# Kernel optimization log

Measured on AMD Instinct MI355X. Metric: run time of the kernel, lower is better.

The kernel has to match this reference:

```python
import jax, jax.numpy as jnp
import numpy as np

B, S, D, H, R, N, KR = 2, 2048, 1024, 16, 256, 8, 128
DH = D // H
EPS = 1e-5


def setup_inputs() -> dict:
    key = jax.random.key(0)
    ks = jax.random.split(key, 20)
    sm = lambda k, n: jax.nn.softmax(jax.random.normal(k, (B, S, n), jnp.float32), axis=-1)
    return {
        "x": jax.random.normal(ks[0], (B, S, D), jnp.float32),
        "fqk_w_Q": sm(ks[1], N),
        "fqk_w_K": sm(ks[2], N),
        "fv_w": sm(ks[3], N),
        "rqk_w_Q": sm(ks[4], N),
        "rqk_w_K": sm(ks[5], N),
        "rv_w": sm(ks[6], N),
        "feature_know_w": sm(ks[7], N),
        "restore_know_w": sm(ks[8], N),
        "f_qk": jax.random.normal(ks[9], (N, D, R), jnp.float32) * 0.02,
        "f_v": jax.random.normal(ks[10], (N, D, R), jnp.float32) * 0.02,
        "r_qk": jax.random.normal(ks[11], (N, R, D), jnp.float32) * 0.02,
        "r_v": jax.random.normal(ks[12], (N, R, D), jnp.float32) * 0.02,
        "f_know": jax.random.normal(ks[13], (N, D, KR), jnp.float32) * 0.02,
        "r_know": jax.random.normal(ks[14], (N, KR, D), jnp.float32) * 0.02,
        "W_O": jax.random.normal(ks[15], (D, D), jnp.float32) * 0.02,
        "ln1_g": jnp.ones((D,), jnp.float32),
        "ln1_b": jnp.zeros((D,), jnp.float32),
        "ln2_g": jnp.ones((D,), jnp.float32),
        "ln2_b": jnp.zeros((D,), jnp.float32),
    }


def _layernorm(x, g, b):
    m = jnp.mean(x, axis=-1, keepdims=True)
    v = jnp.mean(jnp.square(x - m), axis=-1, keepdims=True)
    return (x - m) * jax.lax.rsqrt(v + EPS) * g + b


def _feature(x, neurons, w):
    # fused form of einsum('bsd,ndr->bsnr') + einsum('bsnr,bsn->bsr')
    return jnp.einsum('bsd,bsn,ndr->bsr', x, w, neurons)


def _restore(h, neurons, w):
    # fused form of einsum('bsr,nrd->bsnd') + einsum('bsnd,bsn->bsd')
    return jnp.einsum('bsr,bsn,nrd->bsd', h, w, neurons)


def _causal_sdpa(q, k, v):
    # q,k,v: [B,H,S,DH]
    scores = jnp.einsum('bhqd,bhkd->bhqk', q, k) / jnp.sqrt(jnp.float32(DH))
    mask = jnp.tril(jnp.ones((S, S), bool))
    scores = jnp.where(mask, scores, jnp.finfo(scores.dtype).min)
    p = jax.nn.softmax(scores, axis=-1)
    return jnp.einsum('bhqk,bhkd->bhqd', p, v)


def _block(x, fqk_w_Q, fqk_w_K, fv_w, rqk_w_Q, rqk_w_K, rv_w,
           feature_know_w, restore_know_w, f_qk, f_v, r_qk, r_v,
           f_know, r_know, W_O, ln1_g, ln1_b, ln2_g, ln2_b):
    nx = _layernorm(x, ln1_g, ln1_b)
    h_q = _feature(nx, f_qk, fqk_w_Q)
    h_k = _feature(nx, f_qk, fqk_w_K)
    h_v = _feature(nx, f_v, fv_w)
    Q = _restore(h_q, r_qk, rqk_w_Q)
    K = _restore(h_k, r_qk, rqk_w_K)
    V = _restore(h_v, r_v, rv_w)
    to_heads = lambda t: t.reshape(B, S, H, DH).transpose(0, 2, 1, 3)
    attn = _causal_sdpa(to_heads(Q), to_heads(K), to_heads(V))
    attn = attn.transpose(0, 2, 1, 3).reshape(B, S, D)
    attn_out = attn @ W_O.T  # nn.Linear(d_model,d_model,bias=False)
    x = x + attn_out
    nx2 = _layernorm(x, ln2_g, ln2_b)
    h = _feature(nx2, f_know, feature_know_w)
    know_out = _restore(h, r_know, restore_know_w)
    return x + know_out


def reference(x, fqk_w_Q, fqk_w_K, fv_w, rqk_w_Q, rqk_w_K, rv_w,
              feature_know_w, restore_know_w, f_qk, f_v, r_qk, r_v,
              f_know, r_know, W_O, ln1_g, ln1_b, ln2_g, ln2_b):
    return _block(x, fqk_w_Q, fqk_w_K, fv_w, rqk_w_Q, rqk_w_K, rv_w,
                  feature_know_w, restore_know_w, f_qk, f_v, r_qk, r_v,
                  f_know, r_know, W_O, ln1_g, ln1_b, ln2_g, ln2_b)
```

## Files before the change

### kernel.cpp

```cpp
#include <hip/hip_runtime.h>
#include <hip/hip_bf16.h>


typedef __bf16 bf16_t;
typedef __bf16 bf16x4 __attribute__((ext_vector_type(4)));
typedef __bf16 bf16x8 __attribute__((ext_vector_type(8)));
typedef float f32x4 __attribute__((ext_vector_type(4)));

#define B_DIM 2
#define S_LEN 2048
#define D_DIM 1024
#define H_NUM 16
#define DH 64
#define N_NEU 8
#define R_DIM 256
#define KR_DIM 128
#define ROWS (B_DIM * S_LEN)

static __device__ __forceinline__ void gl_lds16(const void* g, void* l)
{
    __builtin_amdgcn_global_load_lds(
        (__attribute__((address_space(1))) void*)(g),
        (__attribute__((address_space(3))) void*)(l), 16, 0, 0);
}

__global__ __launch_bounds__(256)
void tcast_kernel(const float* __restrict__ in, bf16_t* __restrict__ out, int I, int J)
{
    __shared__ float t[32][33];
    const int bJ = blockIdx.x * 32, bI = blockIdx.y * 32;
    const size_t boff = (size_t)blockIdx.z * I * J;
    const int tx = threadIdx.x, ty = threadIdx.y;
#pragma unroll
    for (int i = 0; i < 4; i++)
        t[ty * 4 + i][tx] = in[boff + (size_t)(bI + ty * 4 + i) * J + bJ + tx];
    __syncthreads();
#pragma unroll
    for (int i = 0; i < 4; i++)
        out[boff + (size_t)(bJ + ty * 4 + i) * I + bI + tx] = (bf16_t)t[tx][ty * 4 + i];
}

__global__ __launch_bounds__(256)
void tbf_kernel(const bf16_t* __restrict__ in, bf16_t* __restrict__ out, int I, int J)
{
    __shared__ bf16_t t[32][33];
    const int bJ = blockIdx.x * 32, bI = blockIdx.y * 32;
    const size_t boff = (size_t)blockIdx.z * I * J;
    const int tx = threadIdx.x, ty = threadIdx.y;
#pragma unroll
    for (int i = 0; i < 4; i++)
        t[ty * 4 + i][tx] = in[boff + (size_t)(bI + ty * 4 + i) * J + bJ + tx];
    __syncthreads();
#pragma unroll
    for (int i = 0; i < 4; i++)
        out[boff + (size_t)(bJ + ty * 4 + i) * I + bI + tx] = t[tx][ty * 4 + i];
}

__global__ __launch_bounds__(256)
void cast_kernel(const float* __restrict__ in, bf16_t* __restrict__ out, int n4)
{
    int i = blockIdx.x * 256 + threadIdx.x;
    if (i < n4) {
        float4 v = ((const float4*)in)[i];
        bf16_t* op = out + (size_t)i * 4;
        op[0] = (bf16_t)v.x; op[1] = (bf16_t)v.y; op[2] = (bf16_t)v.z; op[3] = (bf16_t)v.w;
    }
}

__global__ __launch_bounds__(256)
void ln_kernel(const float* __restrict__ x, const float* __restrict__ g,
               const float* __restrict__ beta, bf16_t* __restrict__ out)
{
    __shared__ float red[4];
    const int row = blockIdx.x;
    const int tid = threadIdx.x;
    float4 v = *(const float4*)&x[(size_t)row * D_DIM + tid * 4];

    float s = v.x + v.y + v.z + v.w;
#pragma unroll
    for (int o = 32; o; o >>= 1) s += __shfl_down(s, o);
    if ((tid & 63) == 0) red[tid >> 6] = s;
    __syncthreads();
    float mean = (red[0] + red[1] + red[2] + red[3]) * (1.f / D_DIM);
    __syncthreads();

    float dx = v.x - mean, dy = v.y - mean, dz = v.z - mean, dw = v.w - mean;
    float q = dx * dx + dy * dy + dz * dz + dw * dw;
#pragma unroll
    for (int o = 32; o; o >>= 1) q += __shfl_down(q, o);
    if ((tid & 63) == 0) red[tid >> 6] = q;
    __syncthreads();
    float var = (red[0] + red[1] + red[2] + red[3]) * (1.f / D_DIM);
    float rstd = rsqrtf(var + 1e-5f);

    float4 gv = *(const float4*)&g[tid * 4];
    float4 bv = *(const float4*)&beta[tid * 4];
    bf16_t* op = out + (size_t)row * D_DIM + tid * 4;
    op[0] = (bf16_t)(dx * rstd * gv.x + bv.x);
    op[1] = (bf16_t)(dy * rstd * gv.y + bv.y);
    op[2] = (bf16_t)(dz * rstd * gv.z + bv.z);
    op[3] = (bf16_t)(dw * rstd * gv.w + bv.w);
}

__global__ __launch_bounds__(256)
void ln2x_kernel(const float* __restrict__ x, const bf16_t* __restrict__ P0,
                 const bf16_t* __restrict__ P1, const float* __restrict__ g,
                 const float* __restrict__ beta, float* __restrict__ outf,
                 bf16_t* __restrict__ outn)
{
    __shared__ float red[4];
    const int row = blockIdx.x;
    const int tid = threadIdx.x;
    const size_t base = (size_t)row * D_DIM + tid * 4;
    float4 v  = *(const float4*)&x[base];
    bf16x4 p0 = *(const bf16x4*)&P0[base];
    bf16x4 p1 = *(const bf16x4*)&P1[base];
    v.x += (float)p0[0] + (float)p1[0];
    v.y += (float)p0[1] + (float)p1[1];
    v.z += (float)p0[2] + (float)p1[2];
    v.w += (float)p0[3] + (float)p1[3];
    *(float4*)&outf[base] = v;

    float s = v.x + v.y + v.z + v.w;
#pragma unroll
    for (int o = 32; o; o >>= 1) s += __shfl_down(s, o);
    if ((tid & 63) == 0) red[tid >> 6] = s;
    __syncthreads();
    float mean = (red[0] + red[1] + red[2] + red[3]) * (1.f / D_DIM);
    __syncthreads();

    float dx = v.x - mean, dy = v.y - mean, dz = v.z - mean, dw = v.w - mean;
    float q = dx * dx + dy * dy + dz * dz + dw * dw;
#pragma unroll
    for (int o = 32; o; o >>= 1) q += __shfl_down(q, o);
    if ((tid & 63) == 0) red[tid >> 6] = q;
    __syncthreads();
    float var = (red[0] + red[1] + red[2] + red[3]) * (1.f / D_DIM);
    float rstd = rsqrtf(var + 1e-5f);

    float4 gv = *(const float4*)&g[tid * 4];
    float4 bv = *(const float4*)&beta[tid * 4];
    bf16_t* op = outn + base;
    op[0] = (bf16_t)(dx * rstd * gv.x + bv.x);
    op[1] = (bf16_t)(dy * rstd * gv.y + bv.y);
    op[2] = (bf16_t)(dz * rstd * gv.z + bv.z);
    op[3] = (bf16_t)(dw * rstd * gv.w + bv.w);
}

__global__ __launch_bounds__(256)
void wsf_kernel(const bf16_t* __restrict__ y,
                const float* __restrict__ wfQ, const float* __restrict__ wrQ,
                const float* __restrict__ wfK, const float* __restrict__ wrK,
                const float* __restrict__ wfV, const float* __restrict__ wrV,
                bf16_t* __restrict__ sq, bf16_t* __restrict__ sk, bf16_t* __restrict__ sv)
{
    const int r = threadIdx.x;
    const int row = blockIdx.x;
    const bf16_t* yrow = y + (size_t)row * 4096;
    const float* fQ = wfQ + row * N_NEU;
    const float* fK = wfK + row * N_NEU;
    const float* fV = wfV + row * N_NEU;
    float aQ = 0.f, aK = 0.f, aV = 0.f;
#pragma unroll
    for (int n = 0; n < N_NEU; n++) {
        float yq = (float)yrow[n * R_DIM + r];
        float yv = (float)yrow[2048 + n * R_DIM + r];
        aQ += fQ[n] * yq;
        aK += fK[n] * yq;
        aV += fV[n] * yv;
    }
    const float* rQ = wrQ + row * N_NEU;
    const float* rK = wrK + row * N_NEU;
    const float* rV = wrV + row * N_NEU;
    const size_t rb = (size_t)row * 2048;
#pragma unroll
    for (int n = 0; n < N_NEU; n++) {
        sq[rb + n * R_DIM + r] = (bf16_t)(rQ[n] * aQ);
        sk[rb + n * R_DIM + r] = (bf16_t)(rK[n] * aK);
        sv[rb + n * R_DIM + r] = (bf16_t)(rV[n] * aV);
    }
}

__global__ __launch_bounds__(256)
void ws2_kernel(const bf16_t* __restrict__ P0, const bf16_t* __restrict__ P1,
                const float* __restrict__ wf, const float* __restrict__ wr,
                bf16_t* __restrict__ sout)
{
    const int lr = threadIdx.x >> 7;
    const int r  = threadIdx.x & 127;
    const int row = blockIdx.x * 2 + lr;
    const size_t rb = (size_t)row * (N_NEU * KR_DIM);
    const float* wfp = wf + row * N_NEU;
    const float* wrp = wr + row * N_NEU;
    float acc = 0.f;
#pragma unroll
    for (int n = 0; n < N_NEU; n++) {
        size_t i = rb + n * KR_DIM + r;
        acc += wfp[n] * ((float)P0[i] + (float)P1[i]);
    }
    bf16_t* srow = sout + rb;
#pragma unroll
    for (int n = 0; n < N_NEU; n++) srow[n * KR_DIM + r] = (bf16_t)(wrp[n] * acc);
}

template<int EPI>
__global__ __launch_bounds__(512, 2)
void gemm256_kernel(const bf16_t* __restrict__ A, const bf16_t* __restrict__ Bt,
                    const bf16_t* __restrict__ Bt2, int splitMy,
                    void* Cout, int M, int N, int K)
{
    __shared__ bf16_t As[3][256][32];
    __shared__ bf16_t Bs[3][128][32];
    const int tid = threadIdx.x;
    const int l = tid & 63, w = tid >> 6;
    const int wr = w >> 1, wc = w & 1;

    const int nbxy = gridDim.x * gridDim.y;
    int bid = blockIdx.y * gridDim.x + blockIdx.x;
    if ((nbxy & 7) == 0) bid = (bid & 7) * (nbxy >> 3) + (bid >> 3);
    const int bx = bid % gridDim.x, by = bid / gridDim.x;

    const int m0 = by * 256, n0 = bx * 128;
    const bf16_t* Bsel = (by < splitMy) ? Bt : Bt2;

    int kbeg = 0, kend = K;
    if constexpr (EPI == 2) { const int half = K >> 1; kbeg = blockIdx.z * half; kend = kbeg + half; }

    const int strow  = w * 16 + (l >> 2);
    const int scelem = ((((l & 3) * 16) ^ ((strow & 6) << 3)) >> 1);
    const bf16_t* Ag0 = A    + (size_t)(m0 + strow) * K + scelem;
    const bf16_t* Ag1 = A    + (size_t)(m0 + strow + 128) * K + scelem;
    const bf16_t* Bg0 = Bsel + (size_t)(n0 + strow) * K + scelem;

    auto stage = [&](int buf, int k0) {
        char* dA = (char*)&As[buf][0][0] + w * 1024;
        char* dB = (char*)&Bs[buf][0][0] + w * 1024;
        gl_lds16(Ag0 + k0, dA);
        gl_lds16(Ag1 + k0, dA + 8192);
        gl_lds16(Bg0 + k0, dB);
    };

    f32x4 acc[4][4];
    const f32x4 zero = {0.f, 0.f, 0.f, 0.f};
#pragma unroll
    for (int i = 0; i < 4; i++)
#pragma unroll
        for (int j = 0; j < 4; j++) acc[i][j] = zero;

    const int fr  = l & 15;
    const int fkb = (l >> 4) * 16;

    stage(0, kbeg);
    stage(1, kbeg + 32);

    const int nK = (kend - kbeg) >> 5;
    for (int it = 0; it < nK; ++it) {
        if (it + 1 < nK) {
            asm volatile("s_waitcnt vmcnt(3)" ::: "memory");
        } else {
            asm volatile("s_waitcnt vmcnt(0)" ::: "memory");
        }
        __builtin_amdgcn_s_barrier();
        __builtin_amdgcn_sched_barrier(0);

        const int cur = it % 3;
        const char* Ab = (const char*)&As[cur][0][0];
        const char* Bb = (const char*)&Bs[cur][0][0];
        bf16x8 af[4], bv[4];
#pragma unroll
        for (int i = 0; i < 4; i++) {
            const int rowA = wr * 64 + i * 16 + fr;
            af[i] = *(const bf16x8*)(Ab + rowA * 64 + (fkb ^ ((rowA & 6) << 3)));
        }
#pragma unroll
        for (int i = 0; i < 4; i++) {
            const int rowB = wc * 64 + i * 16 + fr;
            bv[i] = *(const bf16x8*)(Bb + rowB * 64 + (fkb ^ ((rowB & 6) << 3)));
        }

        if (it + 2 < nK) stage((it + 2) % 3, kbeg + (it + 2) * 32);

        __builtin_amdgcn_s_setprio(1);
#pragma unroll
        for (int mi = 0; mi < 4; mi++)
#pragma unroll
            for (int ni = 0; ni < 4; ni++)
                acc[mi][ni] = __builtin_amdgcn_mfma_f32_16x16x32_bf16(af[mi], bv[ni], acc[mi][ni], 0, 0, 0);
        __builtin_amdgcn_s_setprio(0);
    }

    const int orow = (l >> 4) * 4;
    const int ocol = l & 15;
#pragma unroll
    for (int mi = 0; mi < 4; mi++)
#pragma unroll
        for (int ni = 0; ni < 4; ni++)
#pragma unroll
            for (int j = 0; j < 4; j++) {
                int row = m0 + wr * 64 + mi * 16 + orow + j;
                int col = n0 + wc * 64 + ni * 16 + ocol;
                size_t idx = (size_t)row * N + col;
                if constexpr (EPI == 0) {
                    ((bf16_t*)Cout)[idx] = (bf16_t)acc[mi][ni][j];
                } else {
                    ((bf16_t*)Cout)[(size_t)blockIdx.z * M * N + idx] = (bf16_t)acc[mi][ni][j];
                }
            }
}

template<int EPI>
__global__ __launch_bounds__(256)
void gemm_kernel(const bf16_t* __restrict__ A, const bf16_t* __restrict__ Bt,
                 const bf16_t* __restrict__ Bt2, int splitMy,
                 void* Cout, const float* resid, int M, int N, int K)
{
    __shared__ bf16_t As[3][128][32];
    __shared__ bf16_t Bs[3][128][32];
    const int tid = threadIdx.x;
    const int l = tid & 63, w = tid >> 6;
    const int wr = w >> 1, wc = w & 1;

    const int nbxy = gridDim.x * gridDim.y;
    int bid = blockIdx.y * gridDim.x + blockIdx.x;
    if ((nbxy & 7) == 0) bid = (bid & 7) * (nbxy >> 3) + (bid >> 3);
    const int bx = bid % gridDim.x, by = bid / gridDim.x;

    const int m0 = by * 128, n0 = bx * 128;
    const bf16_t* Bsel = (by < splitMy) ? Bt : Bt2;

    const int kbeg = 0, kend = K;

    const int srow = l >> 2;
    const int scolswz = (((l & 3) * 16) ^ ((srow & 6) << 3)) >> 1;
    const bf16_t* Ag0 = A    + (size_t)(m0 + w * 32 + srow) * K + scolswz;
    const bf16_t* Ag1 = Ag0 + (size_t)16 * K;
    const bf16_t* Bg0 = Bsel + (size_t)(n0 + w * 32 + srow) * K + scolswz;
    const bf16_t* Bg1 = Bg0 + (size_t)16 * K;

    auto stage = [&](int buf, int k0) {
        char* Asb = (char*)&As[buf][0][0] + w * 2048;
        char* Bsb = (char*)&Bs[buf][0][0] + w * 2048;
        gl_lds16(Ag0 + k0, Asb);
        gl_lds16(Ag1 + k0, Asb + 1024);
        gl_lds16(Bg0 + k0, Bsb);
        gl_lds16(Bg1 + k0, Bsb + 1024);
    };

    f32x4 acc[4][4];
    const f32x4 zero = {0.f, 0.f, 0.f, 0.f};
#pragma unroll
    for (int i = 0; i < 4; i++)
#pragma unroll
        for (int j = 0; j < 4; j++) acc[i][j] = zero;

    const int fr = l & 15;
    const int fkb = (l >> 4) * 16;

    stage(0, kbeg);
    stage(1, kbeg + 32);

    const int nK = (kend - kbeg) >> 5;
    for (int it = 0; it < nK; ++it) {
        if (it + 1 < nK) {
            asm volatile("s_waitcnt vmcnt(4)" ::: "memory");
        } else {
            asm volatile("s_waitcnt vmcnt(0)" ::: "memory");
        }
        __builtin_amdgcn_s_barrier();
        __builtin_amdgcn_sched_barrier(0);

        const int cur = it % 3;
        const char* Ab = (const char*)&As[cur][0][0];
        const char* Bb = (const char*)&Bs[cur][0][0];
        bf16x8 af[4], bv[4];
#pragma unroll
        for (int i = 0; i < 4; i++) {
            const int rowA = wr * 64 + i * 16 + fr;
            af[i] = *(const bf16x8*)(Ab + rowA * 64 + (fkb ^ ((rowA & 6) << 3)));
        }
#pragma unroll
        for (int i = 0; i < 4; i++) {
            const int rowB = wc * 64 + i * 16 + fr;
            bv[i] = *(const bf16x8*)(Bb + rowB * 64 + (fkb ^ ((rowB & 6) << 3)));
        }

        if (it + 2 < nK) stage((it + 2) % 3, kbeg + (it + 2) * 32);

        __builtin_amdgcn_s_setprio(1);
#pragma unroll
        for (int mi = 0; mi < 4; mi++)
#pragma unroll
            for (int ni = 0; ni < 4; ni++)
                acc[mi][ni] = __builtin_amdgcn_mfma_f32_16x16x32_bf16(af[mi], bv[ni], acc[mi][ni], 0, 0, 0);
        __builtin_amdgcn_s_setprio(0);
    }

    const int orow = (l >> 4) * 4;
    const int ocol = l & 15;
#pragma unroll
    for (int mi = 0; mi < 4; mi++)
#pragma unroll
        for (int ni = 0; ni < 4; ni++)
#pragma unroll
            for (int j = 0; j < 4; j++) {
                int row = m0 + wr * 64 + mi * 16 + orow + j;
                int col = n0 + wc * 64 + ni * 16 + ocol;
                size_t idx = (size_t)row * N + col;
                if constexpr (EPI == 0) {
                    ((bf16_t*)Cout)[idx] = (bf16_t)acc[mi][ni][j];
                } else {
                    ((float*)Cout)[idx] = acc[mi][ni][j] + resid[idx];
                }
            }
}

__global__ __launch_bounds__(256, 4)
void fa_kernel(const bf16_t* __restrict__ Q, const bf16_t* __restrict__ K,
               const bf16_t* __restrict__ Vt, bf16_t* __restrict__ O)
{
    __shared__ bf16_t Ks[2][64][64];
    __shared__ bf16_t Vs[2][64][64];
    __shared__ bf16_t Ps[4][16][64];

    const int tid = threadIdx.x;
    const int l = tid & 63, w = tid >> 6;

    const int bid  = blockIdx.x;
    const int xcd  = bid & 7;
    const int slot = bid >> 3;
    const int head = slot & 3;
    const int j5   = slot >> 2;
    const int t5   = j5 & 7, u5 = j5 >> 3;
    const int qb   = 8 * u5 + ((u5 & 1) ? (7 - t5) : t5);
    const int bh   = xcd * 4 + head;
    const int b = bh >> 4, h = bh & 15;
    const int q0 = qb * 64;
    const int nt = qb + 1;

    const bf16_t* Qp = Q + (size_t)b * S_LEN * D_DIM + h * DH;
    const bf16_t* Kp = K + (size_t)b * S_LEN * D_DIM + h * DH;
    const bf16_t* Vp = Vt + (size_t)b * D_DIM * S_LEN + (size_t)h * DH * S_LEN;

    const int fr = l & 15, fg = l >> 4, fk = fg * 8;
    const int srow = tid >> 2;
    const int scel = (tid & 3) * 16;
    const int swz  = (srow & 7) << 4;
    const bf16_t* Kst = Kp + (size_t)srow * D_DIM + scel;
    const bf16_t* Vst = Vp + (size_t)srow * S_LEN + scel;

    bf16x8 ones8;
#pragma unroll
    for (int i = 0; i < 8; i++) ones8[i] = (bf16_t)1.f;

    const f32x4 zero = {0.f, 0.f, 0.f, 0.f};
    const float C_LOG2 = 0.125f * 1.44269504f;

    bf16x8 qf[2];
#pragma unroll
    for (int ks = 0; ks < 2; ks++)
        qf[ks] = *(const bf16x8*)(Qp + (size_t)(q0 + w * 16 + fr) * D_DIM + ks * 32 + fk);

    f32x4 o[4];
    f32x4 la = zero;
    float m_r[4];
#pragma unroll
    for (int j = 0; j < 4; j++) { o[j] = zero; m_r[j] = -1e30f; }

    uint4 ka = *(const uint4*)(Kst);
    uint4 kb = *(const uint4*)(Kst + 8);
    uint4 va = *(const uint4*)(Vst);
    uint4 vb = *(const uint4*)(Vst + 8);
    {
        char* kd = (char*)&Ks[0][srow][0];
        char* vd = (char*)&Vs[0][srow][0];
        *(uint4*)(kd + ((scel * 2)      ^ swz)) = ka;
        *(uint4*)(kd + ((scel * 2 + 16) ^ swz)) = kb;
        *(uint4*)(vd + ((scel * 2)      ^ swz)) = va;
        *(uint4*)(vd + ((scel * 2 + 16) ^ swz)) = vb;
    }
    if (nt > 1) {
        ka = *(const uint4*)(Kst + (size_t)64 * D_DIM);
        kb = *(const uint4*)(Kst + (size_t)64 * D_DIM + 8);
        va = *(const uint4*)(Vst + 64);
        vb = *(const uint4*)(Vst + 64 + 8);
    }
    __syncthreads();

    for (int t = 0; t < nt; t++) {
        const int cur = t & 1;

        if (t + 1 < nt) {
            char* kd = (char*)&Ks[cur ^ 1][srow][0];
            char* vd = (char*)&Vs[cur ^ 1][srow][0];
            *(uint4*)(kd + ((scel * 2)      ^ swz)) = ka;
            *(uint4*)(kd + ((scel * 2 + 16) ^ swz)) = kb;
            *(uint4*)(vd + ((scel * 2)      ^ swz)) = va;
            *(uint4*)(vd + ((scel * 2 + 16) ^ swz)) = vb;
        }
        if (t + 2 < nt) {
            const size_t kn = (size_t)(t + 2) * 64;
            ka = *(const uint4*)(Kst + kn * D_DIM);
            kb = *(const uint4*)(Kst + kn * D_DIM + 8);
            va = *(const uint4*)(Vst + kn);
            vb = *(const uint4*)(Vst + kn + 8);
        }

        const int k0 = t * 64;
        f32x4 sc[4];
#pragma unroll
        for (int ni = 0; ni < 4; ni++) sc[ni] = zero;
        __builtin_amdgcn_s_setprio(1);
#pragma unroll
        for (int ks = 0; ks < 2; ks++) {
#pragma unroll
            for (int ni = 0; ni < 4; ni++) {
                const int row = ni * 16 + fr;
                bf16x8 kf = *(const bf16x8*)((const char*)&Ks[cur][row][0]
                              + ((ks * 64 + fg * 16) ^ ((fr & 7) << 4)));
                sc[ni] = __builtin_amdgcn_mfma_f32_16x16x32_bf16(qf[ks], kf, sc[ni], 0, 0, 0);
            }
        }
        __builtin_amdgcn_s_setprio(0);

        float p[4][4];
        if (t == qb) {
#pragma unroll
            for (int ni = 0; ni < 4; ni++) {
                const int key = k0 + ni * 16 + fr;
#pragma unroll
                for (int j = 0; j < 4; j++) {
                    const int qg = q0 + w * 16 + fg * 4 + j;
                    p[ni][j] = (key <= qg) ? sc[ni][j] * C_LOG2 : -1e30f;
                }
            }
        } else {
#pragma unroll
            for (int ni = 0; ni < 4; ni++)
#pragma unroll
                for (int j = 0; j < 4; j++)
                    p[ni][j] = sc[ni][j] * C_LOG2;
        }

#pragma unroll
        for (int j = 0; j < 4; j++) {
            float rmax = fmaxf(fmaxf(p[0][j], p[1][j]), fmaxf(p[2][j], p[3][j]));
#pragma unroll
            for (int d = 1; d < 16; d <<= 1) rmax = fmaxf(rmax, __shfl_xor(rmax, d));
            if (rmax > m_r[j] + 8.f) {
                float scale = exp2f(m_r[j] - rmax);
                la[j] *= scale;
#pragma unroll
                for (int nc = 0; nc < 4; nc++) o[nc][j] *= scale;
                m_r[j] = rmax;
            }
#pragma unroll
            for (int ni = 0; ni < 4; ni++)
                p[ni][j] = exp2f(p[ni][j] - m_r[j]);
        }

#pragma unroll
        for (int ni = 0; ni < 4; ni++)
#pragma unroll
            for (int j = 0; j < 4; j++) {
                const int qrow = fg * 4 + j;
                char* pd = (char*)&Ps[w][qrow][0];
                *(bf16_t*)(pd + (((ni * 16 + fr) * 2) ^ ((qrow & 7) << 4))) = (bf16_t)p[ni][j];
            }

        __builtin_amdgcn_s_setprio(1);
#pragma unroll
        for (int ks = 0; ks < 2; ks++) {
            bf16x8 pa = *(const bf16x8*)((const char*)&Ps[w][fr][0]
                          + ((ks * 64 + fg * 16) ^ ((fr & 7) << 4)));
            la = __builtin_amdgcn_mfma_f32_16x16x32_bf16(pa, ones8, la, 0, 0, 0);
#pragma unroll
            for (int nc = 0; nc < 4; nc++) {
                const int row = nc * 16 + fr;
                bf16x8 vf = *(const bf16x8*)((const char*)&Vs[cur][row][0]
                              + ((ks * 64 + fg * 16) ^ ((fr & 7) << 4)));
                o[nc] = __builtin_amdgcn_mfma_f32_16x16x32_bf16(pa, vf, o[nc], 0, 0, 0);
            }
        }
        __builtin_amdgcn_s_setprio(0);

        __syncthreads();
    }

#pragma unroll
    for (int j = 0; j < 4; j++) {
        const float inv = 1.f / la[j];
        const int q = q0 + w * 16 + fg * 4 + j;
        bf16_t* op = O + (size_t)(b * S_LEN + q) * D_DIM + h * DH;
#pragma unroll
        for (int nc = 0; nc < 4; nc++)
            op[nc * 16 + fr] = (bf16_t)(o[nc][j] * inv);
    }
}

extern "C" void kernel_launch(void* const* d_in, const int* in_sizes, int n_in,
                              void* d_out, int out_size, void* d_ws, size_t ws_size,
                              hipStream_t stream)
{
    const float* x      = (const float*)d_in[0];
    const float* fqk_wQ = (const float*)d_in[1];
    const float* fqk_wK = (const float*)d_in[2];
    const float* fv_w   = (const float*)d_in[3];
    const float* rqk_wQ = (const float*)d_in[4];
    const float* rqk_wK = (const float*)d_in[5];
    const float* rv_w   = (const float*)d_in[6];
    const float* fkn_w  = (const float*)d_in[7];
    const float* rkn_w  = (const float*)d_in[8];
    const float* f_qk   = (const float*)d_in[9];
    const float* f_v    = (const float*)d_in[10];
    const float* r_qk   = (const float*)d_in[11];
    const float* r_v    = (const float*)d_in[12];
    const float* f_know = (const float*)d_in[13];
    const float* r_know = (const float*)d_in[14];
    const float* W_O    = (const float*)d_in[15];
    const float* ln1g   = (const float*)d_in[16];
    const float* ln1b   = (const float*)d_in[17];
    const float* ln2g   = (const float*)d_in[18];
    const float* ln2b   = (const float*)d_in[19];
    float* out_f = (float*)d_out;
    (void)ws_size; (void)in_sizes; (void)n_in; (void)out_size;

    char* ws = (char*)d_ws;
    const size_t MB = 1024 * 1024;
    bf16_t* rqkT   = (bf16_t*)(ws + 0 * MB);
    bf16_t* rvT    = (bf16_t*)(ws + 4 * MB);
    bf16_t* rknT   = (bf16_t*)(ws + 8 * MB);
    bf16_t* woB    = (bf16_t*)(ws + 10 * MB);
    bf16_t* fknT   = (bf16_t*)(ws + 12 * MB);
    bf16_t* buf_nx = (bf16_t*)(ws + 14 * MB);
    bf16_t* buf_y  = (bf16_t*)(ws + 22 * MB);
    char*   buf_s  = ws + 54 * MB;
    bf16_t* fqkT   = (bf16_t*)(buf_s);
    bf16_t* fvT    = (bf16_t*)(buf_s + 4 * MB);
    bf16_t* s_q    = (bf16_t*)(buf_s);
    bf16_t* s_k    = (bf16_t*)(buf_s) + (size_t)4096 * 2048;
    bf16_t* s_v    = (bf16_t*)(buf_s) + (size_t)8192 * 2048;
    bf16_t* attn   = (bf16_t*)(buf_s);
    bf16_t* P0     = (bf16_t*)(buf_s + 16 * MB);
    bf16_t* P0k    = (bf16_t*)(buf_s);
    bf16_t* sk2    = (bf16_t*)(buf_s + 32 * MB);
    bf16_t* Qb     = buf_y;
    bf16_t* Kb     = buf_y + (size_t)4096 * 1024;
    bf16_t* Vb     = buf_y + (size_t)8192 * 1024;
    bf16_t* Vt     = buf_nx;

    const dim3 blk256(256), blk512(512), blkT(32, 8);

    tcast_kernel<<<dim3(R_DIM / 32, D_DIM / 32, N_NEU), blkT, 0, stream>>>(f_qk, fqkT, D_DIM, R_DIM);
    tcast_kernel<<<dim3(R_DIM / 32, D_DIM / 32, N_NEU), blkT, 0, stream>>>(f_v, fvT, D_DIM, R_DIM);
    tcast_kernel<<<dim3(KR_DIM / 32, D_DIM / 32, N_NEU), blkT, 0, stream>>>(f_know, fknT, D_DIM, KR_DIM);
    tcast_kernel<<<dim3(D_DIM / 32, 2048 / 32, 1), blkT, 0, stream>>>(r_qk, rqkT, 2048, D_DIM);
    tcast_kernel<<<dim3(D_DIM / 32, 2048 / 32, 1), blkT, 0, stream>>>(r_v, rvT, 2048, D_DIM);
    tcast_kernel<<<dim3(D_DIM / 32, 1024 / 32, 1), blkT, 0, stream>>>(r_know, rknT, 1024, D_DIM);
    cast_kernel<<<dim3(1024 * 1024 / 4 / 256), blk256, 0, stream>>>(W_O, woB, 1024 * 1024 / 4);

    ln_kernel<<<dim3(ROWS), blk256, 0, stream>>>(x, ln1g, ln1b, buf_nx);

    gemm256_kernel<0><<<dim3(32, 16), blk512, 0, stream>>>(buf_nx, fqkT, fqkT, 1 << 30, buf_y, 4096, 4096, 1024);

    wsf_kernel<<<dim3(ROWS), blk256, 0, stream>>>(buf_y, fqk_wQ, rqk_wQ, fqk_wK, rqk_wK, fv_w, rv_w, s_q, s_k, s_v);

    gemm_kernel<0><<<dim3(8, 96), blk256, 0, stream>>>((bf16_t*)buf_s, rqkT, rvT, 64, buf_y, nullptr, 12288, 1024, 2048);

    tbf_kernel<<<dim3(D_DIM / 32, S_LEN / 32, B_DIM), blkT, 0, stream>>>(Vb, Vt, S_LEN, D_DIM);

    fa_kernel<<<dim3(1024), blk256, 0, stream>>>(Qb, Kb, Vt, attn);

    gemm256_kernel<2><<<dim3(8, 16, 2), blk512, 0, stream>>>(attn, woB, woB, 1 << 30, P0, 4096, 1024, 1024);

    ln2x_kernel<<<dim3(ROWS), blk256, 0, stream>>>(x, P0, P0 + (size_t)4096 * 1024, ln2g, ln2b, out_f, buf_nx);

    gemm256_kernel<2><<<dim3(8, 16, 2), blk512, 0, stream>>>(buf_nx, fknT, fknT, 1 << 30, P0k, 4096, 1024, 1024);

    ws2_kernel<<<dim3(ROWS / 2), blk256, 0, stream>>>(P0k, P0k + (size_t)4096 * 1024, fkn_w, rkn_w, sk2);

    gemm_kernel<1><<<dim3(8, 32), blk256, 0, stream>>>(sk2, rknT, rknT, 1 << 30, d_out, out_f, 4096, 1024, 1024);
}
```

Measured before the change: 315.3 us.

## Enlarge flash-attention tiles to 128 queries and switch restore GEMM to 256-tile kernel

The flash-attention kernel now uses 512-thread blocks covering 128 query rows per block, with paired query-block scheduling for causal load balance. K/V tiles are loaded straight into LDS with global_load_lds, and the previous register-staged double buffer is removed. The online-softmax rescale is skipped wave-wide unless a row max has grown, and the P buffer is padded instead of swizzled. The Q/K/V restore GEMM switches from the 128-tile gemm_kernel to gemm256_kernel; this is meant to improve reuse and latency hiding at the cost of a deeper causal imbalance within blocks and lower occupancy.

```diff
diff --git a/kernel.cpp b/kernel.cpp
--- a/kernel.cpp
+++ b/kernel.cpp
@@ -406,21 +406,17 @@
                 int row = m0 + wr * 64 + mi * 16 + orow + j;
                 int col = n0 + wc * 64 + ni * 16 + ocol;
                 size_t idx = (size_t)row * N + col;
-                if constexpr (EPI == 0) {
-                    ((bf16_t*)Cout)[idx] = (bf16_t)acc[mi][ni][j];
-                } else {
-                    ((float*)Cout)[idx] = acc[mi][ni][j] + resid[idx];
-                }
+                ((float*)Cout)[idx] = acc[mi][ni][j] + resid[idx];
             }
 }
 
-__global__ __launch_bounds__(256, 4)
+__global__ __launch_bounds__(512)
 void fa_kernel(const bf16_t* __restrict__ Q, const bf16_t* __restrict__ K,
                const bf16_t* __restrict__ Vt, bf16_t* __restrict__ O)
 {
     __shared__ bf16_t Ks[2][64][64];
     __shared__ bf16_t Vs[2][64][64];
-    __shared__ bf16_t Ps[4][16][64];
+    __shared__ bf16_t Ps[8][16][72];
 
     const int tid = threadIdx.x;
     const int l = tid & 63, w = tid >> 6;
@@ -429,24 +425,27 @@
     const int xcd  = bid & 7;
     const int slot = bid >> 3;
     const int head = slot & 3;
-    const int j5   = slot >> 2;
-    const int t5   = j5 & 7, u5 = j5 >> 3;
-    const int qb   = 8 * u5 + ((u5 & 1) ? (7 - t5) : t5);
+    const int j16  = slot >> 2;
+    const int p    = (j16 < 8) ? j16 : (23 - j16);
     const int bh   = xcd * 4 + head;
     const int b = bh >> 4, h = bh & 15;
-    const int q0 = qb * 64;
-    const int nt = qb + 1;
+    const int q0 = p * 128;
+    const int nt = 2 * p + 2;
 
     const bf16_t* Qp = Q + (size_t)b * S_LEN * D_DIM + h * DH;
     const bf16_t* Kp = K + (size_t)b * S_LEN * D_DIM + h * DH;
     const bf16_t* Vp = Vt + (size_t)b * D_DIM * S_LEN + (size_t)h * DH * S_LEN;
 
     const int fr = l & 15, fg = l >> 4, fk = fg * 8;
-    const int srow = tid >> 2;
-    const int scel = (tid & 3) * 16;
-    const int swz  = (srow & 7) << 4;
+
+    const int srow = tid >> 3;
+    const int scel = 8 * ((tid & 7) ^ (srow & 7));
     const bf16_t* Kst = Kp + (size_t)srow * D_DIM + scel;
     const bf16_t* Vst = Vp + (size_t)srow * S_LEN + scel;
+    char* KdA = (char*)&Ks[0][w * 8][0];
+    char* KdB = (char*)&Ks[1][w * 8][0];
+    char* VdA = (char*)&Vs[0][w * 8][0];
+    char* VdB = (char*)&Vs[1][w * 8][0];
 
     bf16x8 ones8;
 #pragma unroll
@@ -466,46 +465,27 @@
 #pragma unroll
     for (int j = 0; j < 4; j++) { o[j] = zero; m_r[j] = -1e30f; }
 
-    uint4 ka = *(const uint4*)(Kst);
-    uint4 kb = *(const uint4*)(Kst + 8);
-    uint4 va = *(const uint4*)(Vst);
-    uint4 vb = *(const uint4*)(Vst + 8);
-    {
-        char* kd = (char*)&Ks[0][srow][0];
-        char* vd = (char*)&Vs[0][srow][0];
-        *(uint4*)(kd + ((scel * 2)      ^ swz)) = ka;
-        *(uint4*)(kd + ((scel * 2 + 16) ^ swz)) = kb;
-        *(uint4*)(vd + ((scel * 2)      ^ swz)) = va;
-        *(uint4*)(vd + ((scel * 2 + 16) ^ swz)) = vb;
-    }
-    if (nt > 1) {
-        ka = *(const uint4*)(Kst + (size_t)64 * D_DIM);
-        kb = *(const uint4*)(Kst + (size_t)64 * D_DIM + 8);
-        va = *(const uint4*)(Vst + 64);
-        vb = *(const uint4*)(Vst + 64 + 8);
-    }
-    __syncthreads();
+    const int wq_hi = q0 + w * 16 + 15;
+    const int wq_lo = q0 + w * 16;
+
+    gl_lds16(Kst, KdA);
+    gl_lds16(Vst, VdA);
 
     for (int t = 0; t < nt; t++) {
+        __syncthreads();
+        if (t + 1 < nt) {
+            const size_t kn = (size_t)(t + 1) * 64;
+            gl_lds16(Kst + kn * D_DIM, ((t + 1) & 1) ? KdB : KdA);
+            gl_lds16(Vst + kn,         ((t + 1) & 1) ? VdB : VdA);
+        }
+
+        const int k0 = t * 64;
+        if (k0 > wq_hi) continue;
         const int cur = t & 1;
-
-        if (t + 1 < nt) {
-            char* kd = (char*)&Ks[cur ^ 1][srow][0];
-            char* vd = (char*)&Vs[cur ^ 1][srow][0];
-            *(uint4*)(kd + ((scel * 2)      ^ swz)) = ka;
-            *(uint4*)(kd + ((scel * 2 + 16) ^ swz)) = kb;
-            *(uint4*)(vd + ((scel * 2)      ^ swz)) = va;
-            *(uint4*)(vd + ((scel * 2 + 16) ^ swz)) = vb;
-        }
-        if (t + 2 < nt) {
-            const size_t kn = (size_t)(t + 2) * 64;
-            ka = *(const uint4*)(Kst + kn * D_DIM);
-            kb = *(const uint4*)(Kst + kn * D_DIM + 8);
-            va = *(const uint4*)(Vst + kn);
-            vb = *(const uint4*)(Vst + kn + 8);
-        }
-
-        const int k0 = t * 64;
+        const char* Kb = (const char*)&Ks[cur][0][0];
+        const char* Vb = (const char*)&Vs[cur][0][0];
+        const int rswz = (fr & 7) << 4;
+
         f32x4 sc[4];
 #pragma unroll
         for (int ni = 0; ni < 4; ni++) sc[ni] = zero;
@@ -514,23 +494,22 @@
         for (int ks = 0; ks < 2; ks++) {
 #pragma unroll
             for (int ni = 0; ni < 4; ni++) {
-                const int row = ni * 16 + fr;
-                bf16x8 kf = *(const bf16x8*)((const char*)&Ks[cur][row][0]
-                              + ((ks * 64 + fg * 16) ^ ((fr & 7) << 4)));
+                bf16x8 kf = *(const bf16x8*)(Kb + (ni * 16 + fr) * 128
+                                               + ((ks * 64 + fg * 16) ^ rswz));
                 sc[ni] = __builtin_amdgcn_mfma_f32_16x16x32_bf16(qf[ks], kf, sc[ni], 0, 0, 0);
             }
         }
         __builtin_amdgcn_s_setprio(0);
 
-        float p[4][4];
-        if (t == qb) {
+        float pp[4][4];
+        if (k0 + 63 >= wq_lo) {
 #pragma unroll
             for (int ni = 0; ni < 4; ni++) {
                 const int key = k0 + ni * 16 + fr;
 #pragma unroll
                 for (int j = 0; j < 4; j++) {
-                    const int qg = q0 + w * 16 + fg * 4 + j;
-                    p[ni][j] = (key <= qg) ? sc[ni][j] * C_LOG2 : -1e30f;
+                    const int qg = wq_lo + fg * 4 + j;
+                    pp[ni][j] = (key <= qg) ? sc[ni][j] * C_LOG2 : -1e30f;
                 }
             }
         } else {
@@ -538,58 +517,63 @@
             for (int ni = 0; ni < 4; ni++)
 #pragma unroll
                 for (int j = 0; j < 4; j++)
-                    p[ni][j] = sc[ni][j] * C_LOG2;
-        }
-
+                    pp[ni][j] = sc[ni][j] * C_LOG2;
+        }
+
+        float pmax[4];
 #pragma unroll
         for (int j = 0; j < 4; j++) {
-            float rmax = fmaxf(fmaxf(p[0][j], p[1][j]), fmaxf(p[2][j], p[3][j]));
-#pragma unroll
-            for (int d = 1; d < 16; d <<= 1) rmax = fmaxf(rmax, __shfl_xor(rmax, d));
-            if (rmax > m_r[j] + 8.f) {
-                float scale = exp2f(m_r[j] - rmax);
-                la[j] *= scale;
-#pragma unroll
-                for (int nc = 0; nc < 4; nc++) o[nc][j] *= scale;
-                m_r[j] = rmax;
+            float m8 = fmaxf(fmaxf(pp[0][j], pp[1][j]), fmaxf(pp[2][j], pp[3][j]));
+            pmax[j] = m8;
+        }
+        bool need = (pmax[0] > m_r[0] + 8.f) || (pmax[1] > m_r[1] + 8.f) ||
+                    (pmax[2] > m_r[2] + 8.f) || (pmax[3] > m_r[3] + 8.f);
+        if (__any(need)) {
+#pragma unroll
+            for (int j = 0; j < 4; j++) {
+                float rmax = pmax[j];
+#pragma unroll
+                for (int d = 1; d < 16; d <<= 1) rmax = fmaxf(rmax, __shfl_xor(rmax, d));
+                if (rmax > m_r[j] + 8.f) {
+                    float scale = exp2f(m_r[j] - rmax);
+                    la[j] *= scale;
+#pragma unroll
+                    for (int nc = 0; nc < 4; nc++) o[nc][j] *= scale;
+                    m_r[j] = rmax;
+                }
             }
+        }
+#pragma unroll
+        for (int j = 0; j < 4; j++)
 #pragma unroll
             for (int ni = 0; ni < 4; ni++)
-                p[ni][j] = exp2f(p[ni][j] - m_r[j]);
-        }
+                pp[ni][j] = exp2f(pp[ni][j] - m_r[j]);
 
 #pragma unroll
         for (int ni = 0; ni < 4; ni++)
 #pragma unroll
-            for (int j = 0; j < 4; j++) {
-                const int qrow = fg * 4 + j;
-                char* pd = (char*)&Ps[w][qrow][0];
-                *(bf16_t*)(pd + (((ni * 16 + fr) * 2) ^ ((qrow & 7) << 4))) = (bf16_t)p[ni][j];
-            }
+            for (int j = 0; j < 4; j++)
+                Ps[w][fg * 4 + j][ni * 16 + fr] = (bf16_t)pp[ni][j];
 
         __builtin_amdgcn_s_setprio(1);
 #pragma unroll
         for (int ks = 0; ks < 2; ks++) {
-            bf16x8 pa = *(const bf16x8*)((const char*)&Ps[w][fr][0]
-                          + ((ks * 64 + fg * 16) ^ ((fr & 7) << 4)));
+            bf16x8 pa = *(const bf16x8*)&Ps[w][fr][ks * 32 + fk];
             la = __builtin_amdgcn_mfma_f32_16x16x32_bf16(pa, ones8, la, 0, 0, 0);
 #pragma unroll
             for (int nc = 0; nc < 4; nc++) {
-                const int row = nc * 16 + fr;
-                bf16x8 vf = *(const bf16x8*)((const char*)&Vs[cur][row][0]
-                              + ((ks * 64 + fg * 16) ^ ((fr & 7) << 4)));
+                bf16x8 vf = *(const bf16x8*)(Vb + (nc * 16 + fr) * 128
+                                               + ((ks * 64 + fg * 16) ^ rswz));
                 o[nc] = __builtin_amdgcn_mfma_f32_16x16x32_bf16(pa, vf, o[nc], 0, 0, 0);
             }
         }
         __builtin_amdgcn_s_setprio(0);
-
-        __syncthreads();
     }
 
 #pragma unroll
     for (int j = 0; j < 4; j++) {
         const float inv = 1.f / la[j];
-        const int q = q0 + w * 16 + fg * 4 + j;
+        const int q = wq_lo + fg * 4 + j;
         bf16_t* op = O + (size_t)(b * S_LEN + q) * D_DIM + h * DH;
 #pragma unroll
         for (int nc = 0; nc < 4; nc++)
@@ -664,11 +648,11 @@
 
     wsf_kernel<<<dim3(ROWS), blk256, 0, stream>>>(buf_y, fqk_wQ, rqk_wQ, fqk_wK, rqk_wK, fv_w, rv_w, s_q, s_k, s_v);
 
-    gemm_kernel<0><<<dim3(8, 96), blk256, 0, stream>>>((bf16_t*)buf_s, rqkT, rvT, 64, buf_y, nullptr, 12288, 1024, 2048);
+    gemm256_kernel<0><<<dim3(8, 48), blk512, 0, stream>>>((bf16_t*)buf_s, rqkT, rvT, 32, buf_y, 12288, 1024, 2048);
 
     tbf_kernel<<<dim3(D_DIM / 32, S_LEN / 32, B_DIM), blkT, 0, stream>>>(Vb, Vt, S_LEN, D_DIM);
 
-    fa_kernel<<<dim3(1024), blk256, 0, stream>>>(Qb, Kb, Vt, attn);
+    fa_kernel<<<dim3(512), blk512, 0, stream>>>(Qb, Kb, Vt, attn);
 
     gemm256_kernel<2><<<dim3(8, 16, 2), blk512, 0, stream>>>(attn, woB, woB, 1 << 30, P0, 4096, 1024, 1024);
 
```

New measurement: 277.8 us. -11.9%, faster.
